# Optimization experiments

Hardware: AMD Instinct MI355X
Metric: run time of the kernel (lower is better)

## Reference

```python
import jax, jax.numpy as jnp
import numpy as np
from jax import lax

# Rotation permutations for a flattened 3x3 kernel (row-major, new_flat[t] = orig_flat[perm[t]]),
# transcribed literally from _rotate_kernel for n = angle//45 in {0,1,2,3}.
PERMS = np.array([
    [0, 1, 2, 3, 4, 5, 6, 7, 8],  # 0 deg (identity)
    [3, 0, 1, 6, 4, 2, 7, 8, 5],  # 45 deg: outer ring shifted one step
    [6, 3, 0, 7, 4, 1, 8, 5, 2],  # 90 deg clockwise
    [7, 6, 3, 8, 4, 0, 5, 2, 1],  # 135 deg
], dtype=np.int32)


def setup_inputs() -> dict:
    key = jax.random.key(0)
    k1, k2, k3 = jax.random.split(key, 3)
    B, Cin, Cout, H, W = 16, 64, 64, 128, 128
    x = jax.random.normal(k1, (B, Cin, H, W), dtype=jnp.float32)
    weight = jax.random.normal(k2, (Cout, Cin, 3, 3), dtype=jnp.float32)
    bias = jax.random.normal(k3, (Cout, 1, 1), dtype=jnp.float32)
    return {"x": x, "weight": weight, "bias": bias}


def reference(x, weight, bias):
    # x: [B, Cin, H, W]; weight: [Cout, Cin, 3, 3]; bias: [Cout, 1, 1]
    B, Cin, H, W = x.shape
    Cout = weight.shape[0]
    n_ang = PERMS.shape[0]

    # Build the 4 rotated kernel variants in one gather.
    wflat = weight.reshape(Cout, Cin, 9)
    # [Cout, Cin, n_ang, 9] -> [n_ang, Cout, Cin, 3, 3] -> merge angle into output channels
    wrot = wflat[:, :, jnp.asarray(PERMS)].transpose(2, 0, 1, 3).reshape(n_ang * Cout, Cin, 3, 3)

    # ZeroPad2d(stride=1) then valid 3x3 conv -> same spatial size.
    xp = jnp.pad(x, ((0, 0), (0, 0), (1, 1), (1, 1)))
    y = lax.conv_general_dilated(
        xp, wrot, window_strides=(1, 1), padding="VALID",
        dimension_numbers=("NCHW", "OIHW", "NCHW"))  # [B, n_ang*Cout, H, W]

    y = y.reshape(B, n_ang, Cout, H, W).transpose(1, 0, 2, 3, 4)  # [n_ang, B, Cout, H, W]
    return y + bias  # bias (Cout,1,1) broadcasts over trailing dims
```

## Files before the change

### kernel.cpp

```cpp
#include <hip/hip_runtime.h>


#define CIN 64
#define COUT 64
#define HH 128
#define WW 128
#define NB 16
#define HW (HH*WW)

typedef short bf16x8 __attribute__((ext_vector_type(8)));
typedef float f32x16 __attribute__((ext_vector_type(16)));
#define AS1 __attribute__((address_space(1)))
#define AS3 __attribute__((address_space(3)))

__device__ __constant__ unsigned APERM_d[4][9] = {
  {0,8192,16384,24576,32768,40960,49152,57344,65536},
  {24576,0,8192,49152,32768,16384,57344,65536,40960},
  {49152,24576,0,57344,32768,8192,65536,40960,16384},
  {57344,49152,24576,65536,32768,0,40960,16384,8192},
};

static __device__ __forceinline__ unsigned short f2bf(float f) {
  unsigned u = __builtin_bit_cast(unsigned, f);
  return (unsigned short)((u + 0x7FFFu + ((u >> 16) & 1u)) >> 16);
}
static __device__ __forceinline__ unsigned pk2(float lo, float hi) {
  return (unsigned)f2bf(lo) | ((unsigned)f2bf(hi) << 16);
}

__global__ void build_A_kernel(const float* __restrict__ wgt,
                               unsigned short* __restrict__ A) {
  const int e = blockIdx.x * 256 + threadIdx.x;
  const int j = e & 7;
  const int cm = (e >> 3) & 63;
  const int half = (e >> 9) & 1;
  const int kc = e >> 10;
  const int s = kc >> 2, q = kc & 3;
  const int ci = q * 16 + half * 8 + j;
  A[e] = f2bf(wgt[(cm * CIN + ci) * 9 + s]);
}

static __device__ __forceinline__ void lgkm_barrier() {
  asm volatile("s_waitcnt lgkmcnt(0)" ::: "memory");
  __builtin_amdgcn_s_barrier();
}

#define XS_SLOT 2080
#define XS_ROW  16640
#define XS_OFF  73728
#define LDS_BYTES (XS_OFF + 4 * XS_ROW)

__global__ __launch_bounds__(512) void aconv_v14_kernel(
    const float* __restrict__ x,
    const unsigned short* __restrict__ Ag,
    const float* __restrict__ bias,
    float* __restrict__ out)
{
  __shared__ __align__(16) unsigned char lds[LDS_BYTES];

  const int tid = threadIdx.x;
  const int lane = tid & 63;
  const int wid = tid >> 6;
  const int a   = wid >> 1;
  const int row = wid & 1;
  const int half = lane >> 5;
  const int ln = lane & 31;

  const int b   = blockIdx.x >> 4;
  const int rem = blockIdx.x & 15;
  const int hbase = rem * 8;

  const unsigned char* Agb = (const unsigned char*)Ag;
  AS3 unsigned char* ldsa = (AS3 unsigned char*)lds;
  const uint4 z4 = {0u, 0u, 0u, 0u};

  #pragma unroll
  for (int j = 0; j < 9; ++j) {
    const int i = wid + j * 8;
    __builtin_amdgcn_global_load_lds(
        (const AS1 unsigned*)(Agb + i * 1024 + lane * 16),
        (AS3 unsigned*)(ldsa + i * 1024), 16, 0, 0);
  }

  float bv[2][16];
  #pragma unroll
  for (int mf = 0; mf < 2; ++mf)
    #pragma unroll
    for (int g = 0; g < 16; ++g)
      bv[mf][g] = bias[mf * 32 + (g & 3) + 8 * (g >> 2) + 4 * half];

  #pragma unroll
  for (int i = 0; i < 9; ++i) {
    const int g = tid + i * 512;
    if (g < 4160) {
      const int r    = g / 1040;
      const int rest = g - r * 1040;
      const int slot = rest / 130;
      const int wI   = rest - slot * 130;
      const int gh = hbase - 1 + r;
      const int gw = wI - 1;
      const bool inb = ((unsigned)gh < HH) && ((unsigned)gw < WW);
      const float* xp = x + (size_t)(b * CIN + slot * 8) * HW + (size_t)gh * WW + gw;
      float v[8];
      #pragma unroll
      for (int q = 0; q < 8; ++q) v[q] = inb ? xp[(size_t)q * HW] : 0.f;
      uint4 u;
      u.x = pk2(v[0], v[1]); u.y = pk2(v[2], v[3]);
      u.z = pk2(v[4], v[5]); u.w = pk2(v[6], v[7]);
      *(uint4*)(lds + XS_OFF + r * XS_ROW + slot * XS_SLOT + wI * 16) = u;
    }
  }
  __syncthreads();

  const unsigned char* Asb = lds + (unsigned)(half * 1024 + ln * 16);
  const unsigned char* Bsb = lds + XS_OFF + (unsigned)(half * XS_SLOT + ln * 16);

  float gv[5][8];

  #pragma unroll 1
  for (int ti = 0; ti < 8; ++ti) {
    const int it = ti >> 1;
    const int wh = ti & 1;
    const bool odd = (wh == 1);
    const bool rst = odd && (it < 3);

    unsigned ro[3];
    #pragma unroll
    for (int dh = 0; dh < 3; ++dh)
      ro[dh] = (unsigned)(((it * 2 + row + dh) & 3) * XS_ROW);

    if (rst) {
      #pragma unroll
      for (int i = 0; i < 5; ++i) {
        const int g = tid + i * 512;
        if (g < 2080) {
          const int rr   = g / 1040;
          const int rest = g - rr * 1040;
          const int slot = rest / 130;
          const int wI   = rest - slot * 130;
          const int gh = hbase + it * 2 + 3 + rr;
          const int gw = wI - 1;
          const bool inb = ((unsigned)gh < HH) && ((unsigned)gw < WW);
          const float* xp = x + (size_t)(b * CIN + slot * 8) * HW + (size_t)gh * WW + gw;
          #pragma unroll
          for (int q = 0; q < 8; ++q) gv[i][q] = inb ? xp[(size_t)q * HW] : 0.f;
        }
      }
    }

    f32x16 acc[2][2];
    #pragma unroll
    for (int mf = 0; mf < 2; ++mf)
      #pragma unroll
      for (int nf = 0; nf < 2; ++nf)
        #pragma unroll
        for (int g = 0; g < 16; ++g)
          acc[mf][nf][g] = bv[mf][g];

    const unsigned whb = (unsigned)(wh * 64 * 16);
    #pragma unroll
    for (int t = 0; t < 9; ++t) {
      const unsigned aoff = APERM_d[a][t];
      const unsigned bbt = ro[t / 3] + (unsigned)((t % 3) * 16) + whb;
      #pragma unroll
      for (int q = 0; q < 4; ++q) {
        const bf16x8 af0 = *(const bf16x8*)(Asb + aoff + q * 2048);
        const bf16x8 af1 = *(const bf16x8*)(Asb + aoff + q * 2048 + 512);
        const unsigned bb = bbt + (unsigned)(q * 2 * XS_SLOT);
        const bf16x8 bf0 = *(const bf16x8*)(Bsb + bb);
        const bf16x8 bf1 = *(const bf16x8*)(Bsb + bb + 512);
        acc[0][0] = __builtin_amdgcn_mfma_f32_32x32x16_bf16(af0, bf0, acc[0][0], 0, 0, 0);
        acc[0][1] = __builtin_amdgcn_mfma_f32_32x32x16_bf16(af0, bf1, acc[0][1], 0, 0, 0);
        acc[1][0] = __builtin_amdgcn_mfma_f32_32x32x16_bf16(af1, bf0, acc[1][0], 0, 0, 0);
        acc[1][1] = __builtin_amdgcn_mfma_f32_32x32x16_bf16(af1, bf1, acc[1][1], 0, 0, 0);
      }
    }

    const int hout = hbase + it * 2 + row;
    #pragma unroll
    for (int mf = 0; mf < 2; ++mf)
      #pragma unroll
      for (int nf = 0; nf < 2; ++nf) {
        const f32x16 v = acc[mf][nf];
        float* op = out + (((size_t)(a * NB + b) * COUT + mf * 32 + 4 * half) * HH
                           + hout) * WW + wh * 64 + nf * 32 + ln;
        #pragma unroll
        for (int g = 0; g < 16; ++g)
          __builtin_nontemporal_store(v[g], op + (size_t)((g & 3) + 8 * (g >> 2)) * HW);
      }

    if (rst) {
      lgkm_barrier();
      #pragma unroll
      for (int i = 0; i < 5; ++i) {
        const int g = tid + i * 512;
        if (g < 2080) {
          const int rr   = g / 1040;
          const int rest = g - rr * 1040;
          const int slot = rest / 130;
          const int wI   = rest - slot * 130;
          uint4 u;
          u.x = pk2(gv[i][0], gv[i][1]); u.y = pk2(gv[i][2], gv[i][3]);
          u.z = pk2(gv[i][4], gv[i][5]); u.w = pk2(gv[i][6], gv[i][7]);
          *(uint4*)(lds + XS_OFF + (unsigned)(((it * 2 + 4 + rr) & 3) * XS_ROW)
                    + slot * XS_SLOT + wI * 16) = u;
        }
      }
      lgkm_barrier();
    }
  }
}

extern "C" void kernel_launch(void* const* d_in, const int* in_sizes, int n_in,
                              void* d_out, int out_size, void* d_ws, size_t ws_size,
                              hipStream_t stream) {
  const float* x    = (const float*)d_in[0];
  const float* wgt  = (const float*)d_in[1];
  const float* bias = (const float*)d_in[2];
  float* out = (float*)d_out;
  unsigned short* A = (unsigned short*)d_ws;

  build_A_kernel<<<144, 256, 0, stream>>>(wgt, A);
  aconv_v14_kernel<<<256, 512, 0, stream>>>(x, A, bias, out);
}
```

Baseline: 98.40 us.

## Fold bias into an extra MFMA and issue next-row loads earlier

Bias is no longer held in 32 registers per thread. It is packed into a new bf16 K-chunk of the A matrix and added by one extra MFMA step against a ones vector, which frees VGPRs and drops the bias register initialisation. The prefetch of the next input rows now starts on the even tile and is consumed after the odd tile, so there is more latency hiding. MFMA sections also run at raised wave priority via s_setprio. The bias is now rounded to bf16, which costs accuracy, and the extra MFMAs add a little compute.

```diff
diff --git a/kernel.cpp b/kernel.cpp
--- a/kernel.cpp
+++ b/kernel.cpp
@@ -29,15 +29,20 @@
 }
 
 __global__ void build_A_kernel(const float* __restrict__ wgt,
+                               const float* __restrict__ bias,
                                unsigned short* __restrict__ A) {
   const int e = blockIdx.x * 256 + threadIdx.x;
   const int j = e & 7;
   const int cm = (e >> 3) & 63;
   const int half = (e >> 9) & 1;
   const int kc = e >> 10;
-  const int s = kc >> 2, q = kc & 3;
-  const int ci = q * 16 + half * 8 + j;
-  A[e] = f2bf(wgt[(cm * CIN + ci) * 9 + s]);
+  if (kc < 36) {
+    const int s = kc >> 2, q = kc & 3;
+    const int ci = q * 16 + half * 8 + j;
+    A[e] = f2bf(wgt[(cm * CIN + ci) * 9 + s]);
+  } else if (kc == 36) {
+    A[e] = (half == 0 && j == 0) ? f2bf(bias[cm]) : (unsigned short)0;
+  }
 }
 
 static __device__ __forceinline__ void lgkm_barrier() {
@@ -47,13 +52,12 @@
 
 #define XS_SLOT 2080
 #define XS_ROW  16640
-#define XS_OFF  73728
+#define XS_OFF  75776
 #define LDS_BYTES (XS_OFF + 4 * XS_ROW)
 
-__global__ __launch_bounds__(512) void aconv_v14_kernel(
+__global__ __launch_bounds__(512) void aconv_v15_kernel(
     const float* __restrict__ x,
     const unsigned short* __restrict__ Ag,
-    const float* __restrict__ bias,
     float* __restrict__ out)
 {
   __shared__ __align__(16) unsigned char lds[LDS_BYTES];
@@ -72,22 +76,15 @@
 
   const unsigned char* Agb = (const unsigned char*)Ag;
   AS3 unsigned char* ldsa = (AS3 unsigned char*)lds;
-  const uint4 z4 = {0u, 0u, 0u, 0u};
 
   #pragma unroll
-  for (int j = 0; j < 9; ++j) {
+  for (int j = 0; j < 10; ++j) {
     const int i = wid + j * 8;
-    __builtin_amdgcn_global_load_lds(
-        (const AS1 unsigned*)(Agb + i * 1024 + lane * 16),
-        (AS3 unsigned*)(ldsa + i * 1024), 16, 0, 0);
-  }
-
-  float bv[2][16];
-  #pragma unroll
-  for (int mf = 0; mf < 2; ++mf)
-    #pragma unroll
-    for (int g = 0; g < 16; ++g)
-      bv[mf][g] = bias[mf * 32 + (g & 3) + 8 * (g >> 2) + 4 * half];
+    if (i < 74)
+      __builtin_amdgcn_global_load_lds(
+          (const AS1 unsigned*)(Agb + i * 1024 + lane * 16),
+          (AS3 unsigned*)(ldsa + i * 1024), 16, 0, 0);
+  }
 
   #pragma unroll
   for (int i = 0; i < 9; ++i) {
@@ -115,21 +112,24 @@
   const unsigned char* Asb = lds + (unsigned)(half * 1024 + ln * 16);
   const unsigned char* Bsb = lds + XS_OFF + (unsigned)(half * XS_SLOT + ln * 16);
 
+  bf16x8 ob = (bf16x8)(short)0;
+  if (half == 0) ob[0] = (short)0x3F80;
+
   float gv[5][8];
 
   #pragma unroll 1
   for (int ti = 0; ti < 8; ++ti) {
     const int it = ti >> 1;
     const int wh = ti & 1;
-    const bool odd = (wh == 1);
-    const bool rst = odd && (it < 3);
+    const bool iss = (wh == 0) && (it < 3);
+    const bool rst = (wh == 1) && (it < 3);
 
     unsigned ro[3];
     #pragma unroll
     for (int dh = 0; dh < 3; ++dh)
       ro[dh] = (unsigned)(((it * 2 + row + dh) & 3) * XS_ROW);
 
-    if (rst) {
+    if (iss) {
       #pragma unroll
       for (int i = 0; i < 5; ++i) {
         const int g = tid + i * 512;
@@ -152,12 +152,10 @@
     #pragma unroll
     for (int mf = 0; mf < 2; ++mf)
       #pragma unroll
-      for (int nf = 0; nf < 2; ++nf)
-        #pragma unroll
-        for (int g = 0; g < 16; ++g)
-          acc[mf][nf][g] = bv[mf][g];
+      for (int nf = 0; nf < 2; ++nf) acc[mf][nf] = (f32x16)(0.f);
 
     const unsigned whb = (unsigned)(wh * 64 * 16);
+    __builtin_amdgcn_s_setprio(1);
     #pragma unroll
     for (int t = 0; t < 9; ++t) {
       const unsigned aoff = APERM_d[a][t];
@@ -175,6 +173,15 @@
         acc[1][1] = __builtin_amdgcn_mfma_f32_32x32x16_bf16(af1, bf1, acc[1][1], 0, 0, 0);
       }
     }
+    {
+      const bf16x8 af0 = *(const bf16x8*)(Asb + 36 * 2048);
+      const bf16x8 af1 = *(const bf16x8*)(Asb + 36 * 2048 + 512);
+      acc[0][0] = __builtin_amdgcn_mfma_f32_32x32x16_bf16(af0, ob, acc[0][0], 0, 0, 0);
+      acc[0][1] = __builtin_amdgcn_mfma_f32_32x32x16_bf16(af0, ob, acc[0][1], 0, 0, 0);
+      acc[1][0] = __builtin_amdgcn_mfma_f32_32x32x16_bf16(af1, ob, acc[1][0], 0, 0, 0);
+      acc[1][1] = __builtin_amdgcn_mfma_f32_32x32x16_bf16(af1, ob, acc[1][1], 0, 0, 0);
+    }
+    __builtin_amdgcn_s_setprio(0);
 
     const int hout = hbase + it * 2 + row;
     #pragma unroll
@@ -220,6 +227,6 @@
   float* out = (float*)d_out;
   unsigned short* A = (unsigned short*)d_ws;
 
-  build_A_kernel<<<144, 256, 0, stream>>>(wgt, A);
-  aconv_v14_kernel<<<256, 512, 0, stream>>>(x, A, bias, out);
-}
+  build_A_kernel<<<148, 256, 0, stream>>>(wgt, bias, A);
+  aconv_v15_kernel<<<256, 512, 0, stream>>>(x, A, out);
+}
```

Result: slower. 104.7 us (+6.4%).
